# Kernel optimization log

Hardware: AMD Instinct MI355X
Metric: run time of the kernel (lower is better)

## Reference

```python
import jax, jax.numpy as jnp
import numpy as np

B, S, D = 512, 64, 2048


def setup_inputs() -> dict:
    key = jax.random.key(0)
    ks = jax.random.split(key, 5)
    return {
        "classical_state": jax.random.normal(ks[0], (B, D), jnp.float32),
        "amplitudes": jax.random.normal(ks[1], (S, D), jnp.float32),
        "phases": jax.random.normal(ks[2], (S, D), jnp.float32),
        "rotation_gates": jax.random.normal(ks[3], (S, 2, 2), jnp.float32),
        "entanglement_matrix": jax.random.normal(ks[4], (S, S), jnp.float32),
    }


def reference(classical_state, amplitudes, phases, rotation_gates, entanglement_matrix):
    # classical_state: [B, D]; amplitudes/phases: [S, D]; rotation_gates: [S, 2, 2]
    b, d = classical_state.shape
    s = amplitudes.shape[0]

    # create_superposition
    norm_amp = amplitudes / jnp.linalg.norm(amplitudes, axis=1, keepdims=True)  # F.normalize p=2 dim=1
    real_amp = norm_amp * (jnp.cos(phases) + jnp.sin(phases))                   # [S, D]

    # _apply_quantum_rotation: per-pair (x[:, 2p:2p+2] @ gate) for each gate i -> vectorized over S and pairs
    xr = classical_state.reshape(b, d // 2, 2)                                  # [B, P, 2]
    rotated = jnp.einsum('bpi,sij->bspj', xr, rotation_gates).reshape(b, s, d)  # [B, S, D]

    states = real_amp[None, :, :] * rotated                                     # weighted superposition [B, S, D]

    # _apply_entanglement: softmax over rows then matmul across superposition dim
    ent_w = jax.nn.softmax(entanglement_matrix, axis=1)                          # [S, S]
    entangled = jnp.einsum('st,btd->bsd', ent_w, states)                         # [B, S, D]

    # collapse_superposition: multinomial over softmax(sum of squares), gather selected state
    logits = jnp.sum(entangled * entangled, axis=2)                              # [B, S]
    probabilities = jax.nn.softmax(logits, axis=1)
    outcome = jax.random.categorical(jax.random.key(42), logits, axis=1)         # [B] ~ multinomial(probabilities)
    collapsed = jnp.take_along_axis(entangled, outcome[:, None, None], axis=1)[:, 0, :]  # [B, D]
    return collapsed
```

## Files before the change

### kernel.cpp

```cpp
#include <hip/hip_runtime.h>
#include <math.h>

#define NB 512
#define NS 64
#define ND 2048
#define NP 1024

__device__ __forceinline__ unsigned rotl32(unsigned x, int d) {
    return (x << d) | (x >> (32 - d));
}

__device__ __forceinline__ void threefry2x32(unsigned k0, unsigned k1,
                                             unsigned& x0, unsigned& x1) {
    const unsigned ks0 = k0, ks1 = k1, ks2 = k0 ^ k1 ^ 0x1BD11BDAu;
    const int r0[4] = {13, 15, 26, 6};
    const int r1[4] = {17, 29, 16, 24};
    x0 += ks0; x1 += ks1;
#pragma unroll
    for (int i = 0; i < 4; ++i) { x0 += x1; x1 = rotl32(x1, r0[i]); x1 ^= x0; }
    x0 += ks1; x1 += ks2 + 1u;
#pragma unroll
    for (int i = 0; i < 4; ++i) { x0 += x1; x1 = rotl32(x1, r1[i]); x1 ^= x0; }
    x0 += ks2; x1 += ks0 + 2u;
#pragma unroll
    for (int i = 0; i < 4; ++i) { x0 += x1; x1 = rotl32(x1, r0[i]); x1 ^= x0; }
    x0 += ks0; x1 += ks1 + 3u;
#pragma unroll
    for (int i = 0; i < 4; ++i) { x0 += x1; x1 = rotl32(x1, r1[i]); x1 ^= x0; }
    x0 += ks1; x1 += ks2 + 4u;
#pragma unroll
    for (int i = 0; i < 4; ++i) { x0 += x1; x1 = rotl32(x1, r0[i]); x1 ^= x0; }
    x0 += ks2; x1 += ks0 + 5u;
}

__global__ void __launch_bounds__(1024)
k_MQ(const float* __restrict__ amp, const float* __restrict__ ph,
     const float* __restrict__ G, const float* __restrict__ E,
     float* __restrict__ M0, float* __restrict__ M1, float* __restrict__ Qt) {
    __shared__ float norm2[NS];
    __shared__ float W_l[NS], in_l[NS];
    __shared__ float Gl[NS * 4];
    __shared__ float4 part4[4][256];
    const int blk = blockIdx.x;
    const int tid = threadIdx.x;
    const int srow = blk >> 2;

    {
        const int r = tid >> 4, sub = tid & 15;
        const float4* a4 = (const float4*)(amp + r * ND);
        float acc = 0.f;
#pragma unroll 8
        for (int i = 0; i < 32; ++i) {
            float4 v = a4[sub + 16 * i];
            acc += v.x * v.x + v.y * v.y + v.z * v.z + v.w * v.w;
        }
        acc += __shfl_down(acc, 8, 16);
        acc += __shfl_down(acc, 4, 16);
        acc += __shfl_down(acc, 2, 16);
        acc += __shfl_down(acc, 1, 16);
        if (sub == 0) norm2[r] = acc;
    }
    if (tid < NS * 4) Gl[tid] = G[tid];
    __syncthreads();
    if (tid < NS) {
        in_l[tid] = 1.0f / sqrtf(norm2[tid]);
        float e = E[srow * NS + tid];
        float m = e;
        for (int off = 32; off; off >>= 1) m = fmaxf(m, __shfl_down(m, off));
        m = __shfl(m, 0);
        float ex = expf(e - m);
        float sum = ex;
        for (int off = 32; off; off >>= 1) sum += __shfl_down(sum, off);
        sum = __shfl(sum, 0);
        W_l[tid] = ex / sum;
    }
    __syncthreads();

    {
        const int pi = tid & 255;
        const int tg = tid >> 8;
        const int p = ((blk & 3) << 8) + pi;
        const int t0 = tg << 4;
        const float2* a2 = (const float2*)amp;
        const float2* p2 = (const float2*)ph;
        float a0 = 0.f, a1 = 0.f, b0 = 0.f, b1 = 0.f;
#pragma unroll 4
        for (int t = t0; t < t0 + 16; ++t) {
            float2 av = a2[t * NP + p];
            float2 pv = p2[t * NP + p];
            float w = W_l[t], in = in_l[t];
            float ra0 = av.x * in * (__cosf(pv.x) + __sinf(pv.x));
            float ra1 = av.y * in * (__cosf(pv.y) + __sinf(pv.y));
            float wr0 = w * ra0, wr1 = w * ra1;
            a0 += wr0 * Gl[4 * t + 0];
            b0 += wr0 * Gl[4 * t + 2];
            a1 += wr1 * Gl[4 * t + 1];
            b1 += wr1 * Gl[4 * t + 3];
        }
        part4[tg][pi] = make_float4(a0, a1, b0, b1);
    }
    __syncthreads();

    if (tid < 256) {
        const int p = ((blk & 3) << 8) + tid;
        float4 s0 = part4[0][tid], s1 = part4[1][tid],
               s2 = part4[2][tid], s3 = part4[3][tid];
        float a0 = s0.x + s1.x + s2.x + s3.x;
        float a1 = s0.y + s1.y + s2.y + s3.y;
        float b0 = s0.z + s1.z + s2.z + s3.z;
        float b1 = s0.w + s1.w + s2.w + s3.w;
        float2 m0v = {a0, a1}, m1v = {b0, b1};
        ((float2*)(M0 + srow * ND))[p] = m0v;
        ((float2*)(M1 + srow * ND))[p] = m1v;
        float* qp = Qt + p * 192 + srow * 3;
        qp[0] = a0 * a0 + a1 * a1;
        qp[1] = a0 * b0 + a1 * b1;
        qp[2] = b0 * b0 + b1 * b1;
    }
}

__global__ void __launch_bounds__(1024)
k_row(const float* __restrict__ x, const float* __restrict__ Qt,
      const float* __restrict__ M0, const float* __restrict__ M1,
      float* __restrict__ out) {
    __shared__ float2 xs[2 * NP];
    __shared__ float part[16][2][NS];
    __shared__ int o_sh[2];
    const int blk = blockIdx.x;
    const int tid = threadIdx.x;
    const int r0 = 2 * blk;

    ((float4*)xs)[tid] = ((const float4*)(x + r0 * ND))[tid];
    __syncthreads();

    const int w = tid >> 6, s = tid & 63;
    {
        float acc0 = 0.f, acc1 = 0.f;
        const int p0 = w << 6;
#pragma unroll 4
        for (int p = p0; p < p0 + 64; ++p) {
            const float* qp = Qt + p * 192 + s * 3;
            float q0 = qp[0];
            float q1 = qp[1];
            float q2 = qp[2];
            float2 v0 = xs[p], v1 = xs[NP + p];
            acc0 += v0.x * v0.x * q0 + 2.f * v0.x * v0.y * q1 + v0.y * v0.y * q2;
            acc1 += v1.x * v1.x * q0 + 2.f * v1.x * v1.y * q1 + v1.y * v1.y * q2;
        }
        part[w][0][s] = acc0;
        part[w][1][s] = acc1;
    }
    __syncthreads();

    if (tid < 128) {
        const int w2 = tid >> 6;
        float l = 0.f;
#pragma unroll
        for (int k = 0; k < 16; ++k) l += part[k][w2][s];
        unsigned n = (unsigned)((r0 + w2) * NS + s);
        unsigned t0 = 0u, t1 = n;
        threefry2x32(0u, 42u, t0, t1);
        unsigned bits = t0 ^ t1;
        float u = (float)(bits >> 9) * (1.0f / 8388608.0f);
        u = fmaxf(u, 1.17549435e-38f);
        float g = -logf(-logf(u));
        float best = l + g;
        int bi = s;
        for (int off = 32; off; off >>= 1) {
            float ov = __shfl_down(best, off);
            int oi = __shfl_down(bi, off);
            if (ov > best || (ov == best && oi < bi)) { best = ov; bi = oi; }
        }
        if (s == 0) o_sh[w2] = bi;
    }
    __syncthreads();

#pragma unroll
    for (int r = 0; r < 2; ++r) {
        const int o = o_sh[r];
        const float2* m0p = (const float2*)(M0 + o * ND);
        const float2* m1p = (const float2*)(M1 + o * ND);
        const float2* xr = xs + r * NP;
        float2* op = (float2*)(out + (r0 + r) * ND);
        float2 xv = xr[tid], m0 = m0p[tid], m1 = m1p[tid];
        float2 rr;
        rr.x = xv.x * m0.x + xv.y * m1.x;
        rr.y = xv.x * m0.y + xv.y * m1.y;
        op[tid] = rr;
    }
}

extern "C" void kernel_launch(void* const* d_in, const int* in_sizes, int n_in,
                              void* d_out, int out_size, void* d_ws, size_t ws_size,
                              hipStream_t stream) {
    const float* x   = (const float*)d_in[0];
    const float* amp = (const float*)d_in[1];
    const float* ph  = (const float*)d_in[2];
    const float* G   = (const float*)d_in[3];
    const float* E   = (const float*)d_in[4];
    float* out = (float*)d_out;
    float* ws = (float*)d_ws;

    float* M0 = ws;
    float* M1 = ws + 131072;
    float* Qt = ws + 262144;

    k_MQ <<<256, 1024, 0, stream>>>(amp, ph, G, E, M0, M1, Qt);
    k_row<<<256, 1024, 0, stream>>>(x, Qt, M0, M1, out);
}
```

Baseline: 88.61 us.

## Precompute normalized amplitudes once and batch eight rows per logits block

A new pre-kernel computes the normalized, phase-weighted amplitudes and the softmax weights once, instead of having every k_MQ block redo the norms, sin/cos and softmax. The row kernel now handles eight batch rows per block, split across four P-chunks, so each Qt load is reused eight times. Partial logits go to global memory and an atomic counter picks the last block of each row group, which then samples the outcome and gathers the result. This adds a third launch, a global partial buffer and a fence/atomic synchronization, and the row-rotated loop starts are meant to spread memory accesses.

New measurement: 198.2 us. +123.7%, slower.

```diff
diff --git a/kernel.cpp b/kernel.cpp
--- a/kernel.cpp
+++ b/kernel.cpp
@@ -5,6 +5,14 @@
 #define NS 64
 #define ND 2048
 #define NP 1024
+
+#define OFF_M0   0
+#define OFF_M1   131072
+#define OFF_QT   262144
+#define OFF_R    458752
+#define OFF_W    589824
+#define OFF_PART 593920
+#define OFF_CNT  724992
 
 __device__ __forceinline__ unsigned rotl32(unsigned x, int d) {
     return (x << d) | (x >> (32 - d));
@@ -33,38 +41,33 @@
     x0 += ks2; x1 += ks0 + 5u;
 }
 
-__global__ void __launch_bounds__(1024)
-k_MQ(const float* __restrict__ amp, const float* __restrict__ ph,
-     const float* __restrict__ G, const float* __restrict__ E,
-     float* __restrict__ M0, float* __restrict__ M1, float* __restrict__ Qt) {
-    __shared__ float norm2[NS];
-    __shared__ float W_l[NS], in_l[NS];
-    __shared__ float Gl[NS * 4];
-    __shared__ float4 part4[4][256];
-    const int blk = blockIdx.x;
+__global__ void __launch_bounds__(256)
+k_pre(const float* __restrict__ amp, const float* __restrict__ ph,
+      const float* __restrict__ E, float* __restrict__ R,
+      float* __restrict__ W, int* __restrict__ cnt) {
+    __shared__ float in_sh;
+    const int t = blockIdx.x;
     const int tid = threadIdx.x;
-    const int srow = blk >> 2;
-
-    {
-        const int r = tid >> 4, sub = tid & 15;
-        const float4* a4 = (const float4*)(amp + r * ND);
+
+    if (t == 0 && tid < NS) cnt[tid] = 0;
+
+    if (tid < 16) {
+        const float4* a4 = (const float4*)(amp + t * ND);
         float acc = 0.f;
 #pragma unroll 8
         for (int i = 0; i < 32; ++i) {
-            float4 v = a4[sub + 16 * i];
+            float4 v = a4[tid + 16 * i];
             acc += v.x * v.x + v.y * v.y + v.z * v.z + v.w * v.w;
         }
         acc += __shfl_down(acc, 8, 16);
         acc += __shfl_down(acc, 4, 16);
         acc += __shfl_down(acc, 2, 16);
         acc += __shfl_down(acc, 1, 16);
-        if (sub == 0) norm2[r] = acc;
-    }
-    if (tid < NS * 4) Gl[tid] = G[tid];
-    __syncthreads();
-    if (tid < NS) {
-        in_l[tid] = 1.0f / sqrtf(norm2[tid]);
-        float e = E[srow * NS + tid];
+        if (tid == 0) in_sh = 1.0f / sqrtf(acc);
+    }
+    if (tid >= 64 && tid < 128) {
+        const int s = tid - 64;
+        float e = E[t * NS + s];
         float m = e;
         for (int off = 32; off; off >>= 1) m = fmaxf(m, __shfl_down(m, off));
         m = __shfl(m, 0);
@@ -72,8 +75,38 @@
         float sum = ex;
         for (int off = 32; off; off >>= 1) sum += __shfl_down(sum, off);
         sum = __shfl(sum, 0);
-        W_l[tid] = ex / sum;
-    }
+        W[t * NS + s] = ex / sum;
+    }
+    __syncthreads();
+
+    const float in = in_sh;
+    const float2* a2 = (const float2*)(amp + t * ND);
+    const float2* p2 = (const float2*)(ph + t * ND);
+    float2* r2 = (float2*)(R + t * ND);
+#pragma unroll
+    for (int k = 0; k < 4; ++k) {
+        const int i = tid + 256 * k;
+        float2 av = a2[i], pv = p2[i];
+        float2 rv;
+        rv.x = av.x * in * (__cosf(pv.x) + __sinf(pv.x));
+        rv.y = av.y * in * (__cosf(pv.y) + __sinf(pv.y));
+        r2[i] = rv;
+    }
+}
+
+__global__ void __launch_bounds__(1024)
+k_MQ(const float* __restrict__ R, const float* __restrict__ W,
+     const float* __restrict__ G,
+     float* __restrict__ M0, float* __restrict__ M1, float* __restrict__ Qt) {
+    __shared__ float W_l[NS];
+    __shared__ float Gl[NS * 4];
+    __shared__ float4 part4[4][256];
+    const int blk = blockIdx.x;
+    const int tid = threadIdx.x;
+    const int srow = blk >> 2;
+
+    if (tid < NS) W_l[tid] = W[srow * NS + tid];
+    if (tid >= 256 && tid < 256 + NS * 4) Gl[tid - 256] = G[tid - 256];
     __syncthreads();
 
     {
@@ -81,17 +114,14 @@
         const int tg = tid >> 8;
         const int p = ((blk & 3) << 8) + pi;
         const int t0 = tg << 4;
-        const float2* a2 = (const float2*)amp;
-        const float2* p2 = (const float2*)ph;
+        const float2* r2 = (const float2*)R;
         float a0 = 0.f, a1 = 0.f, b0 = 0.f, b1 = 0.f;
 #pragma unroll 4
-        for (int t = t0; t < t0 + 16; ++t) {
-            float2 av = a2[t * NP + p];
-            float2 pv = p2[t * NP + p];
-            float w = W_l[t], in = in_l[t];
-            float ra0 = av.x * in * (__cosf(pv.x) + __sinf(pv.x));
-            float ra1 = av.y * in * (__cosf(pv.y) + __sinf(pv.y));
-            float wr0 = w * ra0, wr1 = w * ra1;
+        for (int j = 0; j < 16; ++j) {
+            const int t = t0 + ((j + srow) & 15);
+            float2 rv = r2[t * NP + p];
+            float w = W_l[t];
+            float wr0 = w * rv.x, wr1 = w * rv.y;
             a0 += wr0 * Gl[4 * t + 0];
             b0 += wr0 * Gl[4 * t + 2];
             a1 += wr1 * Gl[4 * t + 1];
@@ -120,47 +150,77 @@
 }
 
 __global__ void __launch_bounds__(1024)
-k_row(const float* __restrict__ x, const float* __restrict__ Qt,
+k_log(const float* __restrict__ x, const float* __restrict__ Qt,
       const float* __restrict__ M0, const float* __restrict__ M1,
+      float* __restrict__ pglob, int* __restrict__ cnt,
       float* __restrict__ out) {
-    __shared__ float2 xs[2 * NP];
-    __shared__ float part[16][2][NS];
-    __shared__ int o_sh[2];
+    __shared__ float4 xq[8][256];
+    __shared__ float part[16][8][64];
+    __shared__ int o_sh[8];
+    __shared__ int last_sh;
     const int blk = blockIdx.x;
     const int tid = threadIdx.x;
-    const int r0 = 2 * blk;
-
-    ((float4*)xs)[tid] = ((const float4*)(x + r0 * ND))[tid];
+    const int rg = blk >> 2, pc = blk & 3;
+    const int r0 = rg * 8;
+
+    {
+        const int r = tid >> 7, i = tid & 127;
+        float4 v = ((const float4*)(x + (r0 + r) * ND + pc * 512))[i];
+        float4 q0, q1;
+        q0.x = v.x * v.x; q0.y = 2.f * v.x * v.y; q0.z = v.y * v.y; q0.w = 0.f;
+        q1.x = v.z * v.z; q1.y = 2.f * v.z * v.w; q1.z = v.w * v.w; q1.w = 0.f;
+        xq[r][2 * i] = q0;
+        xq[r][2 * i + 1] = q1;
+    }
     __syncthreads();
 
     const int w = tid >> 6, s = tid & 63;
     {
-        float acc0 = 0.f, acc1 = 0.f;
-        const int p0 = w << 6;
+        float acc[8] = {0.f, 0.f, 0.f, 0.f, 0.f, 0.f, 0.f, 0.f};
+        const float* qbase = Qt + (pc * 256) * 192 + s * 3;
 #pragma unroll 4
-        for (int p = p0; p < p0 + 64; ++p) {
-            const float* qp = Qt + p * 192 + s * 3;
-            float q0 = qp[0];
-            float q1 = qp[1];
-            float q2 = qp[2];
-            float2 v0 = xs[p], v1 = xs[NP + p];
-            acc0 += v0.x * v0.x * q0 + 2.f * v0.x * v0.y * q1 + v0.y * v0.y * q2;
-            acc1 += v1.x * v1.x * q0 + 2.f * v1.x * v1.y * q1 + v1.y * v1.y * q2;
-        }
-        part[w][0][s] = acc0;
-        part[w][1][s] = acc1;
-    }
-    __syncthreads();
-
-    if (tid < 128) {
+        for (int j = 0; j < 16; ++j) {
+            const int pl = (w << 4) + ((j + rg) & 15);
+            const float* qp = qbase + pl * 192;
+            float q0 = qp[0], q1 = qp[1], q2 = qp[2];
+#pragma unroll
+            for (int r = 0; r < 8; ++r) {
+                float4 xv = xq[r][pl];
+                acc[r] += xv.x * q0 + xv.y * q1 + xv.z * q2;
+            }
+        }
+#pragma unroll
+        for (int r = 0; r < 8; ++r) part[w][r][s] = acc[r];
+    }
+    __syncthreads();
+
+    if (tid < 512) {
+        const int rr = tid >> 6;
+        float l = 0.f;
+#pragma unroll
+        for (int k = 0; k < 16; ++k) l += part[k][rr][s];
+        pglob[(pc * NB + r0 + rr) * NS + s] = l;
+    }
+    __threadfence();
+    __syncthreads();
+    if (tid == 0) {
+        int prev = atomicAdd(cnt + rg, 1);
+        last_sh = (prev == 3);
+    }
+    __syncthreads();
+    if (!last_sh) return;
+    __threadfence();
+
+    if (tid < 512) {
         const int w2 = tid >> 6;
+        const int row = r0 + w2;
         float l = 0.f;
 #pragma unroll
-        for (int k = 0; k < 16; ++k) l += part[k][w2][s];
-        unsigned n = (unsigned)((r0 + w2) * NS + s);
-        unsigned t0 = 0u, t1 = n;
-        threefry2x32(0u, 42u, t0, t1);
-        unsigned bits = t0 ^ t1;
+        for (int c = 0; c < 4; ++c) l += pglob[(c * NB + row) * NS + s];
+        unsigned n = (unsigned)(row * NS + s);
+        unsigned t0u = 0u, t1u = n;
+        threefry2x32(0u, 42u, t0u, t1u);
+        unsigned bits = t0u ^ t1u;
         float u = (float)(bits >> 9) * (1.0f / 8388608.0f);
         u = fmaxf(u, 1.17549435e-38f);
         float g = -logf(-logf(u));
@@ -176,17 +236,15 @@
     __syncthreads();
 
 #pragma unroll
-    for (int r = 0; r < 2; ++r) {
+    for (int r = 0; r < 8; ++r) {
         const int o = o_sh[r];
-        const float2* m0p = (const float2*)(M0 + o * ND);
-        const float2* m1p = (const float2*)(M1 + o * ND);
-        const float2* xr = xs + r * NP;
-        float2* op = (float2*)(out + (r0 + r) * ND);
-        float2 xv = xr[tid], m0 = m0p[tid], m1 = m1p[tid];
+        float2 xv = ((const float2*)(x + (r0 + r) * ND))[tid];
+        float2 m0 = ((const float2*)(M0 + o * ND))[tid];
+        float2 m1 = ((const float2*)(M1 + o * ND))[tid];
         float2 rr;
         rr.x = xv.x * m0.x + xv.y * m1.x;
         rr.y = xv.x * m0.y + xv.y * m1.y;
-        op[tid] = rr;
+        ((float2*)(out + (r0 + r) * ND))[tid] = rr;
     }
 }
 
@@ -201,10 +259,15 @@
     float* out = (float*)d_out;
     float* ws = (float*)d_ws;
 
-    float* M0 = ws;
-    float* M1 = ws + 131072;
-    float* Qt = ws + 262144;
-
-    k_MQ <<<256, 1024, 0, stream>>>(amp, ph, G, E, M0, M1, Qt);
-    k_row<<<256, 1024, 0, stream>>>(x, Qt, M0, M1, out);
-}
+    float* M0 = ws + OFF_M0;
+    float* M1 = ws + OFF_M1;
+    float* Qt = ws + OFF_QT;
+    float* R  = ws + OFF_R;
+    float* W  = ws + OFF_W;
+    float* pp = ws + OFF_PART;
+    int*  cnt = (int*)(ws + OFF_CNT);
+
+    k_pre<<<64, 256, 0, stream>>>(amp, ph, E, R, W, cnt);
+    k_MQ <<<256, 1024, 0, stream>>>(R, W, G, M0, M1, Qt);
+    k_log<<<256, 1024, 0, stream>>>(x, Qt, M0, M1, pp, cnt, out);
+}
```

## Pad Qt to float4, process four rows per block, shrink MQ grid

Applied to the files above, without the earlier changes.

Qt is stored as a float4 per (p, s) so each thread in the row kernel loads one vector instead of three scalars. Each row block now handles four batch rows, so every Qt entry is reused across four rows and the grid halves to 128 blocks. The M/Q kernel now uses one block per superposition row that loops over all 64 t, removing the cross-group shared reduction, but it runs only 64 blocks and recomputes the norm/softmax prologue per block. The lower block counts may underfill the GPU's compute units.

Measured after the change: 106.5 us. 1.2x slower.

```diff
diff --git a/kernel.cpp b/kernel.cpp
--- a/kernel.cpp
+++ b/kernel.cpp
@@ -5,6 +5,10 @@
 #define NS 64
 #define ND 2048
 #define NP 1024
+
+#define OFF_M0 0
+#define OFF_M1 131072
+#define OFF_QT 262144
 
 __device__ __forceinline__ unsigned rotl32(unsigned x, int d) {
     return (x << d) | (x >> (32 - d));
@@ -38,12 +42,10 @@
      const float* __restrict__ G, const float* __restrict__ E,
      float* __restrict__ M0, float* __restrict__ M1, float* __restrict__ Qt) {
     __shared__ float norm2[NS];
-    __shared__ float W_l[NS], in_l[NS];
+    __shared__ float in_l[NS], W_l[NS];
     __shared__ float Gl[NS * 4];
-    __shared__ float4 part4[4][256];
-    const int blk = blockIdx.x;
+    const int srow = blockIdx.x;
     const int tid = threadIdx.x;
-    const int srow = blk >> 2;
 
     {
         const int r = tid >> 4, sub = tid & 15;
@@ -76,91 +78,80 @@
     }
     __syncthreads();
 
-    {
-        const int pi = tid & 255;
-        const int tg = tid >> 8;
-        const int p = ((blk & 3) << 8) + pi;
-        const int t0 = tg << 4;
-        const float2* a2 = (const float2*)amp;
-        const float2* p2 = (const float2*)ph;
-        float a0 = 0.f, a1 = 0.f, b0 = 0.f, b1 = 0.f;
+    const int p = tid;
+    const float2* a2 = (const float2*)amp;
+    const float2* p2 = (const float2*)ph;
+    float a0 = 0.f, a1 = 0.f, b0 = 0.f, b1 = 0.f;
 #pragma unroll 4
-        for (int t = t0; t < t0 + 16; ++t) {
-            float2 av = a2[t * NP + p];
-            float2 pv = p2[t * NP + p];
-            float w = W_l[t], in = in_l[t];
-            float ra0 = av.x * in * (__cosf(pv.x) + __sinf(pv.x));
-            float ra1 = av.y * in * (__cosf(pv.y) + __sinf(pv.y));
-            float wr0 = w * ra0, wr1 = w * ra1;
-            a0 += wr0 * Gl[4 * t + 0];
-            b0 += wr0 * Gl[4 * t + 2];
-            a1 += wr1 * Gl[4 * t + 1];
-            b1 += wr1 * Gl[4 * t + 3];
-        }
-        part4[tg][pi] = make_float4(a0, a1, b0, b1);
-    }
-    __syncthreads();
-
-    if (tid < 256) {
-        const int p = ((blk & 3) << 8) + tid;
-        float4 s0 = part4[0][tid], s1 = part4[1][tid],
-               s2 = part4[2][tid], s3 = part4[3][tid];
-        float a0 = s0.x + s1.x + s2.x + s3.x;
-        float a1 = s0.y + s1.y + s2.y + s3.y;
-        float b0 = s0.z + s1.z + s2.z + s3.z;
-        float b1 = s0.w + s1.w + s2.w + s3.w;
-        float2 m0v = {a0, a1}, m1v = {b0, b1};
-        ((float2*)(M0 + srow * ND))[p] = m0v;
-        ((float2*)(M1 + srow * ND))[p] = m1v;
-        float* qp = Qt + p * 192 + srow * 3;
-        qp[0] = a0 * a0 + a1 * a1;
-        qp[1] = a0 * b0 + a1 * b1;
-        qp[2] = b0 * b0 + b1 * b1;
-    }
+    for (int t = 0; t < NS; ++t) {
+        float2 av = a2[t * NP + p];
+        float2 pv = p2[t * NP + p];
+        float in = in_l[t], w = W_l[t];
+        float ra0 = av.x * in * (__cosf(pv.x) + __sinf(pv.x));
+        float ra1 = av.y * in * (__cosf(pv.y) + __sinf(pv.y));
+        float wr0 = w * ra0, wr1 = w * ra1;
+        a0 += wr0 * Gl[4 * t + 0];
+        b0 += wr0 * Gl[4 * t + 2];
+        a1 += wr1 * Gl[4 * t + 1];
+        b1 += wr1 * Gl[4 * t + 3];
+    }
+    ((float2*)(M0 + srow * ND))[p] = make_float2(a0, a1);
+    ((float2*)(M1 + srow * ND))[p] = make_float2(b0, b1);
+    ((float4*)Qt)[p * 64 + srow] =
+        make_float4(a0 * a0 + a1 * a1, a0 * b0 + a1 * b1, b0 * b0 + b1 * b1, 0.f);
 }
 
 __global__ void __launch_bounds__(1024)
-k_row(const float* __restrict__ x, const float* __restrict__ Qt,
+k_out(const float* __restrict__ x, const float* __restrict__ Qt,
       const float* __restrict__ M0, const float* __restrict__ M1,
       float* __restrict__ out) {
-    __shared__ float2 xs[2 * NP];
-    __shared__ float part[16][2][NS];
-    __shared__ int o_sh[2];
-    const int blk = blockIdx.x;
+    __shared__ float2 xs[4][NP];
+    __shared__ float part[16][4][64];
+    __shared__ int o_sh[4];
+    const int rg = blockIdx.x;
     const int tid = threadIdx.x;
-    const int r0 = 2 * blk;
-
-    ((float4*)xs)[tid] = ((const float4*)(x + r0 * ND))[tid];
+    const int r0 = rg * 4;
+
+#pragma unroll
+    for (int k = 0; k < 2; ++k) {
+        const int idx = tid + 1024 * k;
+        const int r = idx >> 9, i = idx & 511;
+        float4 v = ((const float4*)(x + (r0 + r) * ND))[i];
+        xs[r][2 * i]     = make_float2(v.x, v.y);
+        xs[r][2 * i + 1] = make_float2(v.z, v.w);
+    }
     __syncthreads();
 
     const int w = tid >> 6, s = tid & 63;
     {
-        float acc0 = 0.f, acc1 = 0.f;
-        const int p0 = w << 6;
-#pragma unroll 4
-        for (int p = p0; p < p0 + 64; ++p) {
-            const float* qp = Qt + p * 192 + s * 3;
-            float q0 = qp[0];
-            float q1 = qp[1];
-            float q2 = qp[2];
-            float2 v0 = xs[p], v1 = xs[NP + p];
-            acc0 += v0.x * v0.x * q0 + 2.f * v0.x * v0.y * q1 + v0.y * v0.y * q2;
-            acc1 += v1.x * v1.x * q0 + 2.f * v1.x * v1.y * q1 + v1.y * v1.y * q2;
+        float acc[4] = {0.f, 0.f, 0.f, 0.f};
+        const float4* qt4 = (const float4*)Qt + (w << 6) * 64 + s;
+#pragma unroll 8
+        for (int j = 0; j < 64; ++j) {
+            float4 q = qt4[j * 64];
+            const int pl = (w << 6) + j;
+#pragma unroll
+            for (int r = 0; r < 4; ++r) {
+                float2 xv = xs[r][pl];
+                float qx = xv.x * xv.x, qy = 2.f * xv.x * xv.y, qz = xv.y * xv.y;
+                acc[r] += qx * q.x + qy * q.y + qz * q.z;
+            }
         }
-        part[w][0][s] = acc0;
-        part[w][1][s] = acc1;
-    }
-    __syncthreads();
-
-    if (tid < 128) {
-        const int w2 = tid >> 6;
+#pragma unroll
+        for (int r = 0; r < 4; ++r) part[w][r][s] = acc[r];
+    }
+    __syncthreads();
+
+    if (tid < 256) {
+        const int rr = tid >> 6;
+        const int row = r0 + rr;
         float l = 0.f;
 #pragma unroll
-        for (int k = 0; k < 16; ++k) l += part[k][w2][s];
-        unsigned n = (unsigned)((r0 + w2) * NS + s);
-        unsigned t0 = 0u, t1 = n;
-        threefry2x32(0u, 42u, t0, t1);
-        unsigned bits = t0 ^ t1;
+        for (int k = 0; k < 16; ++k) l += part[k][rr][s];
+        unsigned n = (unsigned)(row * NS + s);
+        unsigned t0u = 0u, t1u = n;
+        threefry2x32(0u, 42u, t0u, t1u);
+        unsigned bits = t0u ^ t1u;
         float u = (float)(bits >> 9) * (1.0f / 8388608.0f);
         u = fmaxf(u, 1.17549435e-38f);
         float g = -logf(-logf(u));
@@ -171,22 +162,24 @@
             int oi = __shfl_down(bi, off);
             if (ov > best || (ov == best && oi < bi)) { best = ov; bi = oi; }
         }
-        if (s == 0) o_sh[w2] = bi;
-    }
-    __syncthreads();
-
-#pragma unroll
-    for (int r = 0; r < 2; ++r) {
+        if (s == 0) o_sh[rr] = bi;
+    }
+    __syncthreads();
+
+#pragma unroll
+    for (int k = 0; k < 2; ++k) {
+        const int idx = tid + 1024 * k;
+        const int r = idx >> 9, i = idx & 511;
         const int o = o_sh[r];
-        const float2* m0p = (const float2*)(M0 + o * ND);
-        const float2* m1p = (const float2*)(M1 + o * ND);
-        const float2* xr = xs + r * NP;
-        float2* op = (float2*)(out + (r0 + r) * ND);
-        float2 xv = xr[tid], m0 = m0p[tid], m1 = m1p[tid];
-        float2 rr;
-        rr.x = xv.x * m0.x + xv.y * m1.x;
-        rr.y = xv.x * m0.y + xv.y * m1.y;
-        op[tid] = rr;
+        float2 xa = xs[r][2 * i], xb = xs[r][2 * i + 1];
+        float4 m0 = ((const float4*)(M0 + o * ND))[i];
+        float4 m1 = ((const float4*)(M1 + o * ND))[i];
+        float4 rr4;
+        rr4.x = xa.x * m0.x + xa.y * m1.x;
+        rr4.y = xa.x * m0.y + xa.y * m1.y;
+        rr4.z = xb.x * m0.z + xb.y * m1.z;
+        rr4.w = xb.x * m0.w + xb.y * m1.w;
+        ((float4*)(out + (r0 + r) * ND))[i] = rr4;
     }
 }
 
@@ -201,10 +194,10 @@
     float* out = (float*)d_out;
     float* ws = (float*)d_ws;
 
-    float* M0 = ws;
-    float* M1 = ws + 131072;
-    float* Qt = ws + 262144;
-
-    k_MQ <<<256, 1024, 0, stream>>>(amp, ph, G, E, M0, M1, Qt);
-    k_row<<<256, 1024, 0, stream>>>(x, Qt, M0, M1, out);
-}
+    float* M0 = ws + OFF_M0;
+    float* M1 = ws + OFF_M1;
+    float* Qt = ws + OFF_QT;
+
+    k_MQ <<<64, 1024, 0, stream>>>(amp, ph, G, E, M0, M1, Qt);
+    k_out<<<128, 1024, 0, stream>>>(x, Qt, M0, M1, out);
+}
```
